# Kernel optimization log

Measured on AMD Instinct MI355X. Metric: run time of the kernel, lower is better.

## Reference

```python
import jax, jax.numpy as jnp
import numpy as np

B, T, H = 64, 1024, 1024


def setup_inputs() -> dict:
    key = jax.random.key(0)
    ks = jax.random.split(key, 8)
    s = 1.0 / np.sqrt(H)
    return {
        "spatial_feats": jax.random.normal(ks[0], (B, T, H), dtype=jnp.float32),
        "hidden_state": jax.random.normal(ks[1], (B, H), dtype=jnp.float32),
        "W_enc": jax.random.uniform(ks[2], (H, H), jnp.float32, -s, s),
        "b_enc": jax.random.uniform(ks[3], (H,), jnp.float32, -s, s),
        "W_dec": jax.random.uniform(ks[4], (H, H), jnp.float32, -s, s),
        "b_dec": jax.random.uniform(ks[5], (H,), jnp.float32, -s, s),
        "w_score": jax.random.uniform(ks[6], (H,), jnp.float32, -s, s),
        "b_score": jax.random.uniform(ks[7], (), jnp.float32, -s, s),
    }


def reference(spatial_feats, hidden_state, W_enc, b_enc, W_dec, b_dec, w_score, b_score):
    # decoder_proj(hidden_state): [B, H] -> [B, 1, H]
    dec = (jnp.einsum("bh,oh->bo", hidden_state, W_dec) + b_dec)[:, None, :]
    # encoder_proj(spatial_feats): [B, T, H]
    enc = jnp.einsum("bth,oh->bto", spatial_feats, W_enc) + b_enc
    energy = jnp.tanh(enc + dec)                      # [B, T, H]
    scores = jnp.einsum("bth,h->bt", energy, w_score) + b_score  # [B, T]
    weights = jax.nn.softmax(scores, axis=1)          # [B, T]
    context = jnp.einsum("bth,bt->bh", spatial_feats, weights)   # [B, H]
    return (context, weights)
```

## Files before the change

### kernel.cpp

```cpp
#include <hip/hip_runtime.h>
#include <hip/hip_bf16.h>
#include <math.h>


typedef __attribute__((ext_vector_type(8))) short bf16x8;
typedef __attribute__((ext_vector_type(4))) float f32x4;

__device__ __forceinline__ unsigned short f2bf(float f) {
  union { float f; unsigned int u; } v; v.f = f;
  unsigned int r = v.u + 0x7FFFu + ((v.u >> 16) & 1u);
  return (unsigned short)(r >> 16);
}

__global__ void dec_kernel(const float* __restrict__ hidden,
                           const float* __restrict__ W_dec,
                           const float* __restrict__ b_dec,
                           float* __restrict__ dec) {
  int wave = threadIdx.x >> 6, lane = threadIdx.x & 63;
  int o = blockIdx.x * 4 + wave;
  const float4* hid4 = (const float4*)(hidden + (size_t)lane * 1024);
  const float4* w4   = (const float4*)(W_dec + (size_t)o * 1024);
  float4 acc; acc.x = acc.y = acc.z = acc.w = 0.f;
  #pragma unroll 4
  for (int i = 0; i < 256; i++) {
    float4 x = hid4[i], y = w4[i];
    acc.x = fmaf(x.x, y.x, acc.x);
    acc.y = fmaf(x.y, y.y, acc.y);
    acc.z = fmaf(x.z, y.z, acc.z);
    acc.w = fmaf(x.w, y.w, acc.w);
  }
  dec[lane * 1024 + o] = (acc.x + acc.y) + (acc.z + acc.w) + b_dec[o];
}

__global__ __launch_bounds__(256) void enc_score_kernel(
    const float* __restrict__ A,
    const float* __restrict__ W,
    const float* __restrict__ b_enc,
    const float* __restrict__ dec,
    const float* __restrict__ w_score,
    float* __restrict__ scores)
{
  __shared__ unsigned short As[128][32];
  __shared__ unsigned short Bs[128][32];

  const int bid = blockIdx.x;
  const int n0 = (bid & 7) * 128;
  const int m0 = (bid >> 3) * 128;
  const int tid = threadIdx.x;
  const int lane = tid & 63, wave = tid >> 6;
  const int wm = (wave >> 1) * 64, wn = (wave & 1) * 64;
  const int quad = lane >> 4, col = lane & 15;
  const int srow = tid >> 3;
  const int scol = (tid & 7) * 4;

  f32x4 acc[4][4];
  #pragma unroll
  for (int mi = 0; mi < 4; mi++)
    #pragma unroll
    for (int ni = 0; ni < 4; ni++)
      acc[mi][ni] = (f32x4){0.f, 0.f, 0.f, 0.f};

  for (int k0 = 0; k0 < 1024; k0 += 32) {
    #pragma unroll
    for (int p = 0; p < 4; p++) {
      int r = p * 32 + srow;
      float4 va = *(const float4*)(A + (size_t)(m0 + r) * 1024 + (k0 + scol));
      float4 vb = *(const float4*)(W + (size_t)(n0 + r) * 1024 + (k0 + scol));
      ushort4 pa, pb;
      pa.x = f2bf(va.x); pa.y = f2bf(va.y); pa.z = f2bf(va.z); pa.w = f2bf(va.w);
      pb.x = f2bf(vb.x); pb.y = f2bf(vb.y); pb.z = f2bf(vb.z); pb.w = f2bf(vb.w);
      *(ushort4*)(&As[r][scol]) = pa;
      *(ushort4*)(&Bs[r][scol]) = pb;
    }
    __syncthreads();
    bf16x8 af[4], bfr[4];
    #pragma unroll
    for (int i = 0; i < 4; i++) {
      af[i]  = *(const bf16x8*)(&As[wm + i * 16 + col][quad * 8]);
      bfr[i] = *(const bf16x8*)(&Bs[wn + i * 16 + col][quad * 8]);
    }
    #pragma unroll
    for (int mi = 0; mi < 4; mi++)
      #pragma unroll
      for (int ni = 0; ni < 4; ni++)
        acc[mi][ni] = __builtin_amdgcn_mfma_f32_16x16x32_bf16(
            af[mi], bfr[ni], acc[mi][ni], 0, 0, 0);
    __syncthreads();
  }

  const int b = m0 >> 10;
  float decv[4], wsv[4];
  #pragma unroll
  for (int ni = 0; ni < 4; ni++) {
    int n = n0 + wn + ni * 16 + col;
    decv[ni] = dec[b * 1024 + n] + b_enc[n];
    wsv[ni] = w_score[n];
  }
  #pragma unroll
  for (int mi = 0; mi < 4; mi++) {
    float rs[4] = {0.f, 0.f, 0.f, 0.f};
    #pragma unroll
    for (int ni = 0; ni < 4; ni++)
      #pragma unroll
      for (int r = 0; r < 4; r++)
        rs[r] += tanhf(acc[mi][ni][r] + decv[ni]) * wsv[ni];
    #pragma unroll
    for (int r = 0; r < 4; r++) {
      float v = rs[r];
      v += __shfl_xor(v, 1);
      v += __shfl_xor(v, 2);
      v += __shfl_xor(v, 4);
      v += __shfl_xor(v, 8);
      if (col == 0)
        atomicAdd(&scores[m0 + wm + mi * 16 + quad * 4 + r], v);
    }
  }
}

__global__ void softmax_kernel(const float* __restrict__ scores,
                               float* __restrict__ weights) {
  __shared__ float red[256];
  int b = blockIdx.x, tid = threadIdx.x;
  const float* s = scores + b * 1024;
  float v[4];
  float mx = -1e30f;
  #pragma unroll
  for (int i = 0; i < 4; i++) { v[i] = s[tid + i * 256]; mx = fmaxf(mx, v[i]); }
  red[tid] = mx; __syncthreads();
  for (int off = 128; off > 0; off >>= 1) {
    if (tid < off) red[tid] = fmaxf(red[tid], red[tid + off]);
    __syncthreads();
  }
  mx = red[0]; __syncthreads();
  float sum = 0.f;
  #pragma unroll
  for (int i = 0; i < 4; i++) { v[i] = __expf(v[i] - mx); sum += v[i]; }
  red[tid] = sum; __syncthreads();
  for (int off = 128; off > 0; off >>= 1) {
    if (tid < off) red[tid] += red[tid + off];
    __syncthreads();
  }
  float inv = 1.0f / red[0];
  #pragma unroll
  for (int i = 0; i < 4; i++) weights[b * 1024 + tid + i * 256] = v[i] * inv;
}

__global__ void context_kernel(const float* __restrict__ spatial,
                               const float* __restrict__ weights,
                               float* __restrict__ context) {
  int b = blockIdx.x >> 3, tq = blockIdx.x & 7;
  int tid = threadIdx.x;
  __shared__ float wl[128];
  if (tid < 128) wl[tid] = weights[b * 1024 + tq * 128 + tid];
  __syncthreads();
  const float4* sp =
      (const float4*)(spatial + ((size_t)(b * 1024 + tq * 128)) * 1024);
  float4 acc; acc.x = acc.y = acc.z = acc.w = 0.f;
  #pragma unroll 4
  for (int t = 0; t < 128; t++) {
    float w = wl[t];
    float4 x = sp[(size_t)t * 256 + tid];
    acc.x = fmaf(w, x.x, acc.x);
    acc.y = fmaf(w, x.y, acc.y);
    acc.z = fmaf(w, x.z, acc.z);
    acc.w = fmaf(w, x.w, acc.w);
  }
  float* c = context + b * 1024 + tid * 4;
  atomicAdd(c + 0, acc.x);
  atomicAdd(c + 1, acc.y);
  atomicAdd(c + 2, acc.z);
  atomicAdd(c + 3, acc.w);
}

extern "C" void kernel_launch(void* const* d_in, const int* in_sizes, int n_in,
                              void* d_out, int out_size, void* d_ws, size_t ws_size,
                              hipStream_t stream) {
  const float* spatial  = (const float*)d_in[0];
  const float* hidden   = (const float*)d_in[1];
  const float* W_enc    = (const float*)d_in[2];
  const float* b_enc    = (const float*)d_in[3];
  const float* W_dec    = (const float*)d_in[4];
  const float* b_dec    = (const float*)d_in[5];
  const float* w_score  = (const float*)d_in[6];

  float* out      = (float*)d_out;
  float* context  = out;
  float* weights  = out + 65536;
  float* scores   = (float*)d_ws;
  float* dec      = scores + 65536;

  hipMemsetAsync(scores, 0, 65536 * sizeof(float), stream);
  hipMemsetAsync(context, 0, 65536 * sizeof(float), stream);

  dec_kernel<<<256, 256, 0, stream>>>(hidden, W_dec, b_dec, dec);
  enc_score_kernel<<<4096, 256, 0, stream>>>(spatial, W_enc, b_enc, dec,
                                             w_score, scores);
  softmax_kernel<<<64, 256, 0, stream>>>(scores, weights);
  context_kernel<<<512, 256, 0, stream>>>(spatial, weights, context);
}
```

Baseline: 738.6 us.

## Pre-convert inputs to bf16 and stream GEMM tiles via global_load_lds

Adds a pass that converts spatial_feats and W_enc to bf16 in workspace. The encoder GEMM then loads bf16 tiles straight into LDS with global_load_lds, so per-tile conversion and register staging leave the main loop. The decoder projection is also split over K into four chunks combined with atomics, for more parallelism. The cost is an extra full read of the 256MB input plus a 128MB bf16 write, and the path needs enough workspace, otherwise it falls back to the fp32 kernel.

```diff
diff --git a/kernel.cpp b/kernel.cpp
--- a/kernel.cpp
+++ b/kernel.cpp
@@ -4,12 +4,31 @@
 
 
 typedef __attribute__((ext_vector_type(8))) short bf16x8;
+typedef __attribute__((ext_vector_type(8))) unsigned short ushort8;
 typedef __attribute__((ext_vector_type(4))) float f32x4;
 
 __device__ __forceinline__ unsigned short f2bf(float f) {
   union { float f; unsigned int u; } v; v.f = f;
   unsigned int r = v.u + 0x7FFFu + ((v.u >> 16) & 1u);
   return (unsigned short)(r >> 16);
+}
+
+__device__ __forceinline__ void gld16(const void* g, void* l) {
+  __builtin_amdgcn_global_load_lds(
+      (const __attribute__((address_space(1))) void*)g,
+      (__attribute__((address_space(3))) void*)l, 16, 0, 0);
+}
+
+__global__ void cvt_bf16_kernel(const float* __restrict__ src,
+                                unsigned short* __restrict__ dst, int n8) {
+  int i = blockIdx.x * blockDim.x + threadIdx.x;
+  if (i >= n8) return;
+  const float4* s4 = (const float4*)src;
+  float4 a = s4[(size_t)i * 2], b = s4[(size_t)i * 2 + 1];
+  ushort8 o;
+  o[0] = f2bf(a.x); o[1] = f2bf(a.y); o[2] = f2bf(a.z); o[3] = f2bf(a.w);
+  o[4] = f2bf(b.x); o[5] = f2bf(b.y); o[6] = f2bf(b.z); o[7] = f2bf(b.w);
+  *(ushort8*)(dst + (size_t)i * 8) = o;
 }
 
 __global__ void dec_kernel(const float* __restrict__ hidden,
@@ -17,32 +36,113 @@
                            const float* __restrict__ b_dec,
                            float* __restrict__ dec) {
   int wave = threadIdx.x >> 6, lane = threadIdx.x & 63;
-  int o = blockIdx.x * 4 + wave;
-  const float4* hid4 = (const float4*)(hidden + (size_t)lane * 1024);
-  const float4* w4   = (const float4*)(W_dec + (size_t)o * 1024);
+  int o = (blockIdx.x >> 2) * 4 + wave;
+  int kc = (blockIdx.x & 3) * 256;
+  const float4* hid4 = (const float4*)(hidden + (size_t)lane * 1024 + kc);
+  const float4* w4   = (const float4*)(W_dec + (size_t)o * 1024 + kc);
   float4 acc; acc.x = acc.y = acc.z = acc.w = 0.f;
   #pragma unroll 4
-  for (int i = 0; i < 256; i++) {
+  for (int i = 0; i < 64; i++) {
     float4 x = hid4[i], y = w4[i];
     acc.x = fmaf(x.x, y.x, acc.x);
     acc.y = fmaf(x.y, y.y, acc.y);
     acc.z = fmaf(x.z, y.z, acc.z);
     acc.w = fmaf(x.w, y.w, acc.w);
   }
-  dec[lane * 1024 + o] = (acc.x + acc.y) + (acc.z + acc.w) + b_dec[o];
-}
-
-__global__ __launch_bounds__(256) void enc_score_kernel(
-    const float* __restrict__ A,
-    const float* __restrict__ W,
+  float v = (acc.x + acc.y) + (acc.z + acc.w);
+  if ((blockIdx.x & 3) == 0) v += b_dec[o];
+  atomicAdd(&dec[lane * 1024 + o], v);
+}
+
+__global__ __launch_bounds__(256) void enc_score_bf16_kernel(
+    const unsigned short* __restrict__ A,
+    const unsigned short* __restrict__ W,
     const float* __restrict__ b_enc,
     const float* __restrict__ dec,
     const float* __restrict__ w_score,
     float* __restrict__ scores)
 {
+  __shared__ unsigned short As[128 * 32];
+  __shared__ unsigned short Bs[128 * 32];
+
+  const int bid = blockIdx.x;
+  const int n0 = (bid & 7) * 128;
+  const int m0 = (bid >> 3) * 128;
+  const int tid = threadIdx.x;
+  const int lane = tid & 63, wave = tid >> 6;
+  const int wm = (wave >> 1) * 64, wn = (wave & 1) * 64;
+  const int quad = lane >> 4, col = lane & 15;
+
+  const int srow = wave * 32 + (lane >> 2);
+  const int scol = (lane & 3) * 8;
+  const unsigned short* ga = A + (size_t)(m0 + srow) * 1024 + scol;
+  const unsigned short* gb = W + (size_t)(n0 + srow) * 1024 + scol;
+  unsigned short* la = As + wave * 32 * 32;
+  unsigned short* lb = Bs + wave * 32 * 32;
+
+  f32x4 acc[4][4];
+  #pragma unroll
+  for (int mi = 0; mi < 4; mi++)
+    #pragma unroll
+    for (int ni = 0; ni < 4; ni++)
+      acc[mi][ni] = (f32x4){0.f, 0.f, 0.f, 0.f};
+
+  for (int k0 = 0; k0 < 1024; k0 += 32) {
+    gld16(ga + k0,             la);
+    gld16(ga + k0 + 16 * 1024, la + 16 * 32);
+    gld16(gb + k0,             lb);
+    gld16(gb + k0 + 16 * 1024, lb + 16 * 32);
+    __syncthreads();
+    bf16x8 af[4], bfr[4];
+    #pragma unroll
+    for (int i = 0; i < 4; i++) {
+      af[i]  = *(const bf16x8*)(As + (wm + i * 16 + col) * 32 + quad * 8);
+      bfr[i] = *(const bf16x8*)(Bs + (wn + i * 16 + col) * 32 + quad * 8);
+    }
+    #pragma unroll
+    for (int mi = 0; mi < 4; mi++)
+      #pragma unroll
+      for (int ni = 0; ni < 4; ni++)
+        acc[mi][ni] = __builtin_amdgcn_mfma_f32_16x16x32_bf16(
+            af[mi], bfr[ni], acc[mi][ni], 0, 0, 0);
+    __syncthreads();
+  }
+
+  const int b = m0 >> 10;
+  float decv[4], wsv[4];
+  #pragma unroll
+  for (int ni = 0; ni < 4; ni++) {
+    int n = n0 + wn + ni * 16 + col;
+    decv[ni] = dec[b * 1024 + n] + b_enc[n];
+    wsv[ni] = w_score[n];
+  }
+  #pragma unroll
+  for (int mi = 0; mi < 4; mi++) {
+    float rs[4] = {0.f, 0.f, 0.f, 0.f};
+    #pragma unroll
+    for (int ni = 0; ni < 4; ni++)
+      #pragma unroll
+      for (int r = 0; r < 4; r++)
+        rs[r] += tanhf(acc[mi][ni][r] + decv[ni]) * wsv[ni];
+    #pragma unroll
+    for (int r = 0; r < 4; r++) {
+      float v = rs[r];
+      v += __shfl_xor(v, 1);
+      v += __shfl_xor(v, 2);
+      v += __shfl_xor(v, 4);
+      v += __shfl_xor(v, 8);
+      if (col == 0)
+        atomicAdd(&scores[m0 + wm + mi * 16 + quad * 4 + r], v);
+    }
+  }
+}
+
+__global__ __launch_bounds__(256) void enc_score_f32_kernel(
+    const float* __restrict__ A, const float* __restrict__ W,
+    const float* __restrict__ b_enc, const float* __restrict__ dec,
+    const float* __restrict__ w_score, float* __restrict__ scores) {
   __shared__ unsigned short As[128][32];
   __shared__ unsigned short Bs[128][32];
-
   const int bid = blockIdx.x;
   const int n0 = (bid & 7) * 128;
   const int m0 = (bid >> 3) * 128;
@@ -52,14 +152,12 @@
   const int quad = lane >> 4, col = lane & 15;
   const int srow = tid >> 3;
   const int scol = (tid & 7) * 4;
-
   f32x4 acc[4][4];
   #pragma unroll
   for (int mi = 0; mi < 4; mi++)
     #pragma unroll
     for (int ni = 0; ni < 4; ni++)
       acc[mi][ni] = (f32x4){0.f, 0.f, 0.f, 0.f};
-
   for (int k0 = 0; k0 < 1024; k0 += 32) {
     #pragma unroll
     for (int p = 0; p < 4; p++) {
@@ -87,7 +185,6 @@
             af[mi], bfr[ni], acc[mi][ni], 0, 0, 0);
     __syncthreads();
   }
-
   const int b = m0 >> 10;
   float decv[4], wsv[4];
   #pragma unroll
@@ -186,15 +283,29 @@
   float* out      = (float*)d_out;
   float* context  = out;
   float* weights  = out + 65536;
+
   float* scores   = (float*)d_ws;
   float* dec      = scores + 65536;
-
-  hipMemsetAsync(scores, 0, 65536 * sizeof(float), stream);
+  unsigned short* Wbf = (unsigned short*)(dec + 65536);
+  unsigned short* Abf = Wbf + 1024 * 1024;
+
+  const size_t need = 512 * 1024 + 2ull * 1024 * 1024 + 2ull * 65536 * 1024;
+
+  hipMemsetAsync(scores, 0, 2 * 65536 * sizeof(float), stream);
   hipMemsetAsync(context, 0, 65536 * sizeof(float), stream);
 
-  dec_kernel<<<256, 256, 0, stream>>>(hidden, W_dec, b_dec, dec);
-  enc_score_kernel<<<4096, 256, 0, stream>>>(spatial, W_enc, b_enc, dec,
-                                             w_score, scores);
+  dec_kernel<<<1024, 256, 0, stream>>>(hidden, W_dec, b_dec, dec);
+
+  if (ws_size >= need) {
+    cvt_bf16_kernel<<<512, 256, 0, stream>>>(W_enc, Wbf, 1024 * 1024 / 8);
+    cvt_bf16_kernel<<<32768, 256, 0, stream>>>(spatial, Abf, 65536 * 1024 / 8);
+    enc_score_bf16_kernel<<<4096, 256, 0, stream>>>(Abf, Wbf, b_enc, dec,
+                                                    w_score, scores);
+  } else {
+    enc_score_f32_kernel<<<4096, 256, 0, stream>>>(spatial, W_enc, b_enc, dec,
+                                                   w_score, scores);
+  }
+
   softmax_kernel<<<64, 256, 0, stream>>>(scores, weights);
   context_kernel<<<512, 256, 0, stream>>>(spatial, weights, context);
 }
```

After: 702.9 us. 1.05x faster.
